# Performance work log

Hardware: AMD Instinct MI355X
Metric: run time of the kernel (lower is better)

The kernel has to match this reference:

```python
import jax, jax.numpy as jnp
import numpy as np

H = 128
B, N, K = 2, 16384, 16


def _gather_neighbors(a, idx):
    # a: (B,N,D), idx: (B,N,K) -> (B,N,K,D), per-batch gather along N
    return jax.vmap(lambda ab, ib: ab[ib])(a, idx)


def setup_inputs() -> dict:
    key = jax.random.key(0)
    ks = jax.random.split(key, 16)
    def lin(k, fan_in, shape):
        lim = 1.0 / np.sqrt(fan_in)
        return jax.random.uniform(k, shape, jnp.float32, -lim, lim)
    inp = {
        'h': jax.random.normal(ks[0], (B, N, H), jnp.float32),
        'x': jax.random.normal(ks[1], (B, N, 3), jnp.float32),
        'edge_idx': jax.random.randint(ks[2], (B, N, K), 0, N),
        # edge_mlp: Linear(2H+1->H), SiLU, Linear(H->H), SiLU
        'We1': lin(ks[3], 2 * H + 1, (2 * H + 1, H)), 'be1': lin(ks[4], 2 * H + 1, (H,)),
        'We2': lin(ks[5], H, (H, H)), 'be2': lin(ks[6], H, (H,)),
        # coord_mlp: Linear(H->H), SiLU, Linear(H->1, no bias)
        'Wc1': lin(ks[7], H, (H, H)), 'bc1': lin(ks[8], H, (H,)),
        'Wc2': lin(ks[9], H, (H, 1)),
        # node_mlp: Linear(2H->H), SiLU, Linear(H->H)
        'Wn1': lin(ks[10], 2 * H, (2 * H, H)), 'bn1': lin(ks[11], 2 * H, (H,)),
        'Wn2': lin(ks[12], H, (H, H)), 'bn2': lin(ks[13], H, (H,)),
    }
    return inp


def reference(h, x, edge_idx, We1, be1, We2, be2, Wc1, bc1, Wc2, Wn1, bn1, Wn2, bn2):
    k = edge_idx.shape[2]
    h_neigh = _gather_neighbors(h, edge_idx)          # (B,N,K,H)
    x_neigh = _gather_neighbors(x, edge_idx)          # (B,N,K,3)
    x_diff = x[:, :, None, :] - x_neigh               # (B,N,K,3)
    sq_dist = jnp.sum(x_diff * x_diff, axis=-1, keepdims=True)  # (B,N,K,1)
    h_i = jnp.broadcast_to(h[:, :, None, :], h_neigh.shape)
    edge_feat = jnp.concatenate([h_i, h_neigh, sq_dist], axis=-1)  # (B,N,K,2H+1)
    m_ij = jax.nn.silu(jax.nn.silu(edge_feat @ We1 + be1) @ We2 + be2)  # (B,N,K,H)
    coord_w = jax.nn.silu(m_ij @ Wc1 + bc1) @ Wc2     # (B,N,K,1)
    x_new = x + jnp.mean(x_diff * coord_w, axis=2)    # (B,N,3)
    m_i = jnp.sum(m_ij, axis=2)                       # (B,N,H)
    node_in = jnp.concatenate([h, m_i], axis=-1)      # (B,N,2H)
    h_new = jax.nn.silu(node_in @ Wn1 + bn1) @ Wn2 + bn2 + h
    return (h_new, x_new)
```

## Files before the change

### kernel.cpp

```cpp
#include <hip/hip_runtime.h>
#include <hip/hip_bf16.h>
#include <math.h>

#define H 128
#define KN 16
#define NN 16384
#define NB 8
#define EB 128
#define HS 136

typedef short s16x8 __attribute__((ext_vector_type(8)));
typedef float f32x4 __attribute__((ext_vector_type(4)));

__device__ __forceinline__ float u2f_lo(uint u){
    union { uint i; float f; } v; v.i = u << 16; return v.f;
}
__device__ __forceinline__ float u2f_hi(uint u){
    union { uint i; float f; } v; v.i = u & 0xffff0000u; return v.f;
}
__device__ __forceinline__ uint pk2(float lo, float hi){
    __hip_bfloat162 b = __float22bfloat162_rn(float2{lo, hi});
    uint u; __builtin_memcpy(&u, &b, 4); return u;
}
__device__ __forceinline__ ushort f2b1(float f){
    __hip_bfloat16 b = __float2bfloat16(f);
    ushort u; __builtin_memcpy(&u, &b, 2); return u;
}
__device__ __forceinline__ float silu_f(float v){
    float e = __expf(-v);
    return v * __builtin_amdgcn_rcpf(1.0f + e);
}

__global__ __launch_bounds__(256) void pack_all(
    const float* __restrict__ We2, const float* __restrict__ Wc1,
    const float* __restrict__ Wn1, const float* __restrict__ Wn2,
    const float* __restrict__ We1,
    ushort* __restrict__ dWe2, ushort* __restrict__ dWc1,
    ushort* __restrict__ dWn1, ushort* __restrict__ dWn2,
    ushort* __restrict__ dW1p)
{
    int idx = blockIdx.x * 256 + threadIdx.x;
    int fid = idx >> 6, l = idx & 63;
    const float* src; ushort* dst; int Kt; int mode = 0; int lfid;
    if (fid < 32)       { src = We2; dst = dWe2; Kt = 4; lfid = fid; }
    else if (fid < 64)  { src = Wc1; dst = dWc1; Kt = 4; lfid = fid - 32; }
    else if (fid < 128) { src = Wn1; dst = dWn1; Kt = 8; lfid = fid - 64; }
    else if (fid < 160) { src = Wn2; dst = dWn2; Kt = 4; lfid = fid - 128; }
    else                { src = We1; dst = dW1p; Kt = 4; mode = 1; lfid = fid - 160; }
    int mt = lfid / Kt, kt = lfid % Kt;
    int m = mt * 16 + (l & 15);
    s16x8 ov;
#pragma unroll
    for (int e = 0; e < 8; e++){
        int k = kt * 32 + ((l >> 4) << 3) + e;
        float v;
        if (mode == 0) v = src[k * 128 + m];
        else           v = src[(k + ((m >= 128) ? 128 : 0)) * 128 + (m & 127)];
        ov[e] = (short)f2b1(v);
    }
    *(s16x8*)(dst + (size_t)lfid * 512 + l * 8) = ov;
}

__global__ __launch_bounds__(256) void precompute_mfma(
    const float* __restrict__ h, const float* __restrict__ be1,
    const ushort* __restrict__ W1p,
    ushort* __restrict__ A, ushort* __restrict__ Bm)
{
    const int tid = threadIdx.x;
    const int w = tid >> 6, l = tid & 63, lg = l >> 4, li = l & 15;
    const int i0 = blockIdx.x * 64;

    f32x4 acc[4][4];
#pragma unroll
    for (int a = 0; a < 4; a++)
#pragma unroll
        for (int b = 0; b < 4; b++){ acc[a][b][0]=0.f; acc[a][b][1]=0.f; acc[a][b][2]=0.f; acc[a][b][3]=0.f; }

    for (int nt = 0; nt < 4; nt++){
        int node = i0 + nt * 16 + li;
        const float* hp = h + (size_t)node * 128 + lg * 8;
        s16x8 bfr[4];
#pragma unroll
        for (int kt = 0; kt < 4; kt++){
            float4 v0 = *(const float4*)(hp + kt * 32);
            float4 v1 = *(const float4*)(hp + kt * 32 + 4);
            uint4 uu = make_uint4(pk2(v0.x, v0.y), pk2(v0.z, v0.w),
                                  pk2(v1.x, v1.y), pk2(v1.z, v1.w));
            s16x8 bf; __builtin_memcpy(&bf, &uu, 16);
            bfr[kt] = bf;
        }
#pragma unroll
        for (int mtl = 0; mtl < 4; mtl++){
            int mt = w * 4 + mtl;
#pragma unroll
            for (int kt = 0; kt < 4; kt++){
                s16x8 af = *(const s16x8*)(W1p + (size_t)(mt * 4 + kt) * 512 + l * 8);
                acc[mtl][nt] = __builtin_amdgcn_mfma_f32_16x16x32_bf16(af, bfr[kt], acc[mtl][nt], 0, 0, 0);
            }
        }
    }
#pragma unroll
    for (int mtl = 0; mtl < 4; mtl++){
        int mt = w * 4 + mtl;
        int ccb = mt * 16 + lg * 4;
#pragma unroll
        for (int nt = 0; nt < 4; nt++){
            int node = i0 + nt * 16 + li;
            float b0=0.f,b1=0.f,b2=0.f,b3=0.f;
            if (ccb < 128){ float4 bb = *(const float4*)(be1 + ccb); b0=bb.x; b1=bb.y; b2=bb.z; b3=bb.w; }
            uint2 val = make_uint2(pk2(acc[mtl][nt][0] + b0, acc[mtl][nt][1] + b1),
                                   pk2(acc[mtl][nt][2] + b2, acc[mtl][nt][3] + b3));
            ushort* dst = (ccb < 128) ? (A + (size_t)node * 128 + ccb)
                                      : (Bm + (size_t)node * 128 + (ccb - 128));
            *(uint2*)dst = val;
        }
    }
}

__global__ __launch_bounds__(256, 3) void egnn_fused(
    const float* __restrict__ h, const float* __restrict__ x,
    const int* __restrict__ edge_idx,
    const ushort* __restrict__ A, const ushort* __restrict__ Bm,
    const float* __restrict__ We1,
    const ushort* __restrict__ We2T, const float* __restrict__ be2,
    const ushort* __restrict__ Wc1T, const float* __restrict__ bc1,
    const float* __restrict__ Wc2,
    const ushort* __restrict__ Wn1T, const float* __restrict__ bn1,
    const ushort* __restrict__ Wn2T, const float* __restrict__ bn2,
    float* __restrict__ out, int BN)
{
    __shared__ __align__(16) ushort m_lds[EB * 128];
    __shared__ __align__(16) uint   AshCw[512];
    __shared__ __align__(16) ushort hsh_bf[NB * HS];
    __shared__ __align__(16) ushort msum_bf[NB * HS];
    __shared__ __align__(16) ushort w256sh[128];
    __shared__ float  sqd[EB];
    __shared__ float  xd[EB * 3];
    __shared__ int    jgs[EB];

    ushort* Ash = (ushort*)AshCw;
    float (*cwvp)[EB] = (float(*)[EB])AshCw;

    const int tid = threadIdx.x;
    const int w = tid >> 6, l = tid & 63, lg = l >> 4, li = l & 15;
    const int i0 = blockIdx.x * NB;

    {
        int r = tid >> 5, c = (tid & 31) * 4;
        float4 hv = *(const float4*)&h[(size_t)(i0 + r) * 128 + c];
        *(uint2*)&hsh_bf[r * HS + c] = make_uint2(pk2(hv.x, hv.y), pk2(hv.z, hv.w));
        if (tid < 128){
            int rr = tid >> 4, cc = (tid & 15) * 8;
            *(uint4*)&Ash[rr * 128 + cc] = *(const uint4*)&A[(size_t)(i0 + rr) * 128 + cc];
        } else {
            int t2 = tid - 128;
            w256sh[t2] = f2b1(We1[256 * 128 + t2]);
        }
        if (tid < EB){
            int e = tid;
            int i = i0 + (e >> 4);
            int b = i / NN;
            int jl = edge_idx[(size_t)i * KN + (e & 15)];
            int j = b * NN + jl;
            jgs[e] = j;
            float d0 = x[(size_t)i*3+0] - x[(size_t)j*3+0];
            float d1 = x[(size_t)i*3+1] - x[(size_t)j*3+1];
            float d2 = x[(size_t)i*3+2] - x[(size_t)j*3+2];
            xd[e*3+0] = d0; xd[e*3+1] = d1; xd[e*3+2] = d2;
            sqd[e] = d0*d0 + d1*d1 + d2*d2;
        }
    }
    __syncthreads();

    {
        const int e0 = w * 32;
#pragma unroll
        for (int nt = 0; nt < 2; nt++){
            int edge = e0 + nt * 16 + li;
            int nodel = edge >> 4;
            int j = jgs[edge];
            float sq = sqd[edge];
#pragma unroll
            for (int kt = 0; kt < 4; kt++){
                int c8 = kt * 32 + lg * 8;
                uint4 ub = *(const uint4*)&Bm[(size_t)j * 128 + c8];
                uint4 ua = *(const uint4*)&Ash[nodel * 128 + c8];
                uint4 uw = *(const uint4*)&w256sh[c8];
                uint ov[4];
                const uint* pa = (const uint*)&ua;
                const uint* pb = (const uint*)&ub;
                const uint* pw = (const uint*)&uw;
#pragma unroll
                for (int p = 0; p < 4; p++){
                    float tlo = fmaf(sq, u2f_lo(pw[p]), u2f_lo(pa[p]) + u2f_lo(pb[p]));
                    float thi = fmaf(sq, u2f_hi(pw[p]), u2f_hi(pa[p]) + u2f_hi(pb[p]));
                    ov[p] = pk2(silu_f(tlo), silu_f(thi));
                }
                int blk = (kt * 4 + lg) ^ (edge & 7);
                *(uint4*)&m_lds[edge * 128 + blk * 8] = make_uint4(ov[0], ov[1], ov[2], ov[3]);
            }
        }
    }
    __syncthreads();

    f32x4 acc[16];
#pragma unroll
    for (int q = 0; q < 16; q++){ acc[q][0]=0.f; acc[q][1]=0.f; acc[q][2]=0.f; acc[q][3]=0.f; }

    __builtin_amdgcn_s_setprio(1);
#pragma unroll
    for (int kt = 0; kt < 4; kt++){
        s16x8 bfr[8];
#pragma unroll
        for (int nt = 0; nt < 8; nt++){
            int edge = nt * 16 + li;
            int blk = (kt * 4 + lg) ^ (edge & 7);
            bfr[nt] = *(const s16x8*)&m_lds[edge * 128 + blk * 8];
        }
#pragma unroll
        for (int mtl = 0; mtl < 2; mtl++){
            int mt = w * 2 + mtl;
            s16x8 af = *(const s16x8*)&We2T[(size_t)(mt * 4 + kt) * 512 + l * 8];
#pragma unroll
            for (int nt = 0; nt < 8; nt++)
                acc[mtl * 8 + nt] = __builtin_amdgcn_mfma_f32_16x16x32_bf16(af, bfr[nt], acc[mtl * 8 + nt], 0, 0, 0);
        }
    }
    __builtin_amdgcn_s_setprio(0);
    __syncthreads();

#pragma unroll
    for (int mtl = 0; mtl < 2; mtl++){
        int mt = w * 2 + mtl;
        int cb = mt * 16 + lg * 4;
        float4 bb = *(const float4*)&be2[cb];
#pragma unroll
        for (int nt = 0; nt < 8; nt++){
            int edge = nt * 16 + li;
            f32x4 a = acc[mtl * 8 + nt];
            uint2 val = make_uint2(pk2(silu_f(a[0] + bb.x), silu_f(a[1] + bb.y)),
                                   pk2(silu_f(a[2] + bb.z), silu_f(a[3] + bb.w)));
            int blk = (mt * 2 + (lg >> 1)) ^ (edge & 7);
            *(uint2*)&m_lds[edge * 128 + blk * 8 + (lg & 1) * 4] = val;
        }
    }
    __syncthreads();
    {
        int nodel = l >> 3;
        int c0 = w * 32 + (l & 7) * 4;
        float s0=0.f, s1=0.f, s2=0.f, s3=0.f;
#pragma unroll
        for (int k = 0; k < 16; k++){
            int edge = nodel * 16 + k;
            int blk = (c0 >> 3) ^ (edge & 7);
            uint2 v = *(uint2*)&m_lds[edge * 128 + blk * 8 + (c0 & 4)];
            s0 += u2f_lo(v.x); s1 += u2f_hi(v.x);
            s2 += u2f_lo(v.y); s3 += u2f_hi(v.y);
        }
        *(uint2*)&msum_bf[nodel * HS + c0] = make_uint2(pk2(s0, s1), pk2(s2, s3));
    }
    __syncthreads();

#pragma unroll
    for (int q = 0; q < 16; q++){ acc[q][0]=0.f; acc[q][1]=0.f; acc[q][2]=0.f; acc[q][3]=0.f; }
    __builtin_amdgcn_s_setprio(1);
#pragma unroll
    for (int kt = 0; kt < 4; kt++){
        s16x8 bfr[8];
#pragma unroll
        for (int nt = 0; nt < 8; nt++){
            int edge = nt * 16 + li;
            int blk = (kt * 4 + lg) ^ (edge & 7);
            bfr[nt] = *(const s16x8*)&m_lds[edge * 128 + blk * 8];
        }
#pragma unroll
        for (int mtl = 0; mtl < 2; mtl++){
            int mt = w * 2 + mtl;
            s16x8 af = *(const s16x8*)&Wc1T[(size_t)(mt * 4 + kt) * 512 + l * 8];
#pragma unroll
            for (int nt = 0; nt < 8; nt++)
                acc[mtl * 8 + nt] = __builtin_amdgcn_mfma_f32_16x16x32_bf16(af, bfr[nt], acc[mtl * 8 + nt], 0, 0, 0);
        }
    }
    __builtin_amdgcn_s_setprio(0);
    __syncthreads();

    {
        float cwp[8];
#pragma unroll
        for (int nt = 0; nt < 8; nt++) cwp[nt] = 0.f;
#pragma unroll
        for (int mtl = 0; mtl < 2; mtl++){
            int mt = w * 2 + mtl;
            int cb = mt * 16 + lg * 4;
            float4 bc = *(const float4*)&bc1[cb];
            float4 wc = *(const float4*)&Wc2[cb];
#pragma unroll
            for (int nt = 0; nt < 8; nt++){
                f32x4 a = acc[mtl * 8 + nt];
                cwp[nt] += silu_f(a[0] + bc.x) * wc.x + silu_f(a[1] + bc.y) * wc.y
                         + silu_f(a[2] + bc.z) * wc.z + silu_f(a[3] + bc.w) * wc.w;
            }
        }
#pragma unroll
        for (int nt = 0; nt < 8; nt++){
            float v = cwp[nt];
            v += __shfl_xor(v, 16);
            v += __shfl_xor(v, 32);
            if (lg == 0) cwvp[w][nt * 16 + li] = v;
        }
    }

    {
        f32x4 acc3[2];
        acc3[0][0]=0.f; acc3[0][1]=0.f; acc3[0][2]=0.f; acc3[0][3]=0.f;
        acc3[1][0]=0.f; acc3[1][1]=0.f; acc3[1][2]=0.f; acc3[1][3]=0.f;
        int node = li & 7;
#pragma unroll
        for (int kt = 0; kt < 8; kt++){
            const ushort* bp = (kt < 4) ? &hsh_bf[node * HS + kt * 32 + lg * 8]
                                        : &msum_bf[node * HS + (kt - 4) * 32 + lg * 8];
            s16x8 bf = *(const s16x8*)bp;
#pragma unroll
            for (int mtl = 0; mtl < 2; mtl++){
                int mt = w * 2 + mtl;
                s16x8 af = *(const s16x8*)&Wn1T[(size_t)(mt * 8 + kt) * 512 + l * 8];
                acc3[mtl] = __builtin_amdgcn_mfma_f32_16x16x32_bf16(af, bf, acc3[mtl], 0, 0, 0);
            }
        }
#pragma unroll
        for (int mtl = 0; mtl < 2; mtl++){
            int mt = w * 2 + mtl;
            int cb = mt * 16 + lg * 4;
            float4 bb = *(const float4*)&bn1[cb];
            uint o01 = 0, o23 = 0;
            if (li < 8){
                f32x4 a = acc3[mtl];
                o01 = pk2(silu_f(a[0] + bb.x), silu_f(a[1] + bb.y));
                o23 = pk2(silu_f(a[2] + bb.z), silu_f(a[3] + bb.w));
            }
            int blk = (mt * 2 + (lg >> 1)) ^ (li & 7);
            *(uint2*)&m_lds[li * 128 + blk * 8 + (lg & 1) * 4] = make_uint2(o01, o23);
        }
    }
    __syncthreads();

    if (tid < 24){
        int nd = tid / 3, d = tid % 3;
        int i = i0 + nd;
        float s = 0.f;
#pragma unroll
        for (int k = 0; k < 16; k++){
            int e = nd * 16 + k;
            float cw = cwvp[0][e] + cwvp[1][e] + cwvp[2][e] + cwvp[3][e];
            s += xd[e * 3 + d] * cw;
        }
        out[(size_t)BN * H + (size_t)i * 3 + d] = x[(size_t)i * 3 + d] + s * (1.0f / 16.0f);
    }

    {
        f32x4 acc4[2];
        acc4[0][0]=0.f; acc4[0][1]=0.f; acc4[0][2]=0.f; acc4[0][3]=0.f;
        acc4[1][0]=0.f; acc4[1][1]=0.f; acc4[1][2]=0.f; acc4[1][3]=0.f;
#pragma unroll
        for (int kt = 0; kt < 4; kt++){
            int blk = (kt * 4 + lg) ^ (li & 7);
            s16x8 bf = *(const s16x8*)&m_lds[li * 128 + blk * 8];
#pragma unroll
            for (int mtl = 0; mtl < 2; mtl++){
                int mt = w * 2 + mtl;
                s16x8 af = *(const s16x8*)&Wn2T[(size_t)(mt * 4 + kt) * 512 + l * 8];
                acc4[mtl] = __builtin_amdgcn_mfma_f32_16x16x32_bf16(af, bf, acc4[mtl], 0, 0, 0);
            }
        }
#pragma unroll
        for (int mtl = 0; mtl < 2; mtl++){
            int mt = w * 2 + mtl;
            int cb = mt * 16 + lg * 4;
            if (li < 8){
                float4 bb = *(const float4*)&bn2[cb];
                uint2 hu = *(const uint2*)&hsh_bf[li * HS + cb];
                f32x4 a = acc4[mtl];
                float4 o;
                o.x = a[0] + bb.x + u2f_lo(hu.x);
                o.y = a[1] + bb.y + u2f_hi(hu.x);
                o.z = a[2] + bb.z + u2f_lo(hu.y);
                o.w = a[3] + bb.w + u2f_hi(hu.y);
                *(float4*)&out[(size_t)(i0 + li) * 128 + cb] = o;
            }
        }
    }
}

extern "C" void kernel_launch(void* const* d_in, const int* in_sizes, int n_in,
                              void* d_out, int out_size, void* d_ws, size_t ws_size,
                              hipStream_t stream) {
    const float* h        = (const float*)d_in[0];
    const float* x        = (const float*)d_in[1];
    const int*   edge_idx = (const int*)d_in[2];
    const float* We1      = (const float*)d_in[3];
    const float* be1      = (const float*)d_in[4];
    const float* We2      = (const float*)d_in[5];
    const float* be2      = (const float*)d_in[6];
    const float* Wc1      = (const float*)d_in[7];
    const float* bc1      = (const float*)d_in[8];
    const float* Wc2      = (const float*)d_in[9];
    const float* Wn1      = (const float*)d_in[10];
    const float* bn1      = (const float*)d_in[11];
    const float* Wn2      = (const float*)d_in[12];
    const float* bn2      = (const float*)d_in[13];
    float* out = (float*)d_out;

    const int BN = in_sizes[0] / H;

    ushort* A    = (ushort*)d_ws;
    ushort* Bm   = A + (size_t)BN * H;
    ushort* We2T = Bm + (size_t)BN * H;
    ushort* Wc1T = We2T + 32 * 512;
    ushort* Wn1T = Wc1T + 32 * 512;
    ushort* Wn2T = Wn1T + 64 * 512;
    ushort* W1pT = Wn2T + 32 * 512;

    pack_all<<<56, 256, 0, stream>>>(We2, Wc1, Wn1, Wn2, We1,
                                     We2T, Wc1T, Wn1T, Wn2T, W1pT);
    precompute_mfma<<<BN / 64, 256, 0, stream>>>(h, be1, W1pT, A, Bm);
    egnn_fused<<<BN / NB, 256, 0, stream>>>(h, x, edge_idx, A, Bm, We1,
                                            We2T, be2, Wc1T, bc1, Wc2,
                                            Wn1T, bn1, Wn2T, bn2, out, BN);
}
```

Measured before the change: 125.1 us.

## Split edge GEMMs into half-width passes and shrink LDS to raise occupancy

```diff
diff --git a/kernel.cpp b/kernel.cpp
--- a/kernel.cpp
+++ b/kernel.cpp
@@ -17,6 +17,9 @@
 }
 __device__ __forceinline__ float u2f_hi(uint u){
     union { uint i; float f; } v; v.i = u & 0xffff0000u; return v.f;
+}
+__device__ __forceinline__ float b2f(ushort u){
+    union { uint i; float f; } v; v.i = ((uint)u) << 16; return v.f;
 }
 __device__ __forceinline__ uint pk2(float lo, float hi){
     __hip_bfloat162 b = __float22bfloat162_rn(float2{lo, hi});
@@ -117,7 +120,88 @@
     }
 }
 
-__global__ __launch_bounds__(256, 3) void egnn_fused(
+__device__ __forceinline__ void gemm_pass(
+    const ushort* mlds, const ushort* __restrict__ WT,
+    int nt0, int w, int l, int lg, int li, f32x4 acc[2][4])
+{
+#pragma unroll
+    for (int kt = 0; kt < 4; kt++){
+        s16x8 bfr[4];
+#pragma unroll
+        for (int n = 0; n < 4; n++){
+            int edge = (nt0 + n) * 16 + li;
+            int blk = (kt * 4 + lg) ^ (edge & 7);
+            bfr[n] = *(const s16x8*)&mlds[edge * 128 + blk * 8];
+        }
+#pragma unroll
+        for (int mtl = 0; mtl < 2; mtl++){
+            s16x8 af = *(const s16x8*)&WT[(size_t)((w * 2 + mtl) * 4 + kt) * 512 + l * 8];
+#pragma unroll
+            for (int n = 0; n < 4; n++)
+                acc[mtl][n] = __builtin_amdgcn_mfma_f32_16x16x32_bf16(af, bfr[n], acc[mtl][n], 0, 0, 0);
+        }
+    }
+}
+
+__device__ __forceinline__ void m_epi(
+    ushort* mlds, const float* __restrict__ be2,
+    int nt0, int w, int lg, int li, f32x4 acc[2][4])
+{
+#pragma unroll
+    for (int mtl = 0; mtl < 2; mtl++){
+        int mt = w * 2 + mtl;
+        int cb = mt * 16 + lg * 4;
+        float4 bb = *(const float4*)&be2[cb];
+#pragma unroll
+        for (int n = 0; n < 4; n++){
+            int el = (nt0 + n) * 16 + li;
+            f32x4 a = acc[mtl][n];
+            uint2 val = make_uint2(pk2(silu_f(a[0] + bb.x), silu_f(a[1] + bb.y)),
+                                   pk2(silu_f(a[2] + bb.z), silu_f(a[3] + bb.w)));
+            int blk = (mt * 2 + (lg >> 1)) ^ (el & 7);
+            *(uint2*)&mlds[el * 128 + blk * 8 + (lg & 1) * 4] = val;
+        }
+    }
+}
+
+__device__ __forceinline__ void gemm2_pass(
+    const ushort* mlds, const ushort* __restrict__ WT,
+    const float* __restrict__ bc1, const float* __restrict__ Wc2,
+    float* cwrow, int nt0, int w, int l, int lg, int li)
+{
+    f32x4 acc[2][4];
+#pragma unroll
+    for (int m = 0; m < 2; m++)
+#pragma unroll
+        for (int n = 0; n < 4; n++){ acc[m][n][0]=0.f; acc[m][n][1]=0.f; acc[m][n][2]=0.f; acc[m][n][3]=0.f; }
+
+    __builtin_amdgcn_s_setprio(1);
+    gemm_pass(mlds, WT, nt0, w, l, lg, li, acc);
+    __builtin_amdgcn_s_setprio(0);
+
+    float cwp[4] = {0.f, 0.f, 0.f, 0.f};
+#pragma unroll
+    for (int mtl = 0; mtl < 2; mtl++){
+        int cb = (w * 2 + mtl) * 16 + lg * 4;
+        float4 bc = *(const float4*)&bc1[cb];
+        float4 wc = *(const float4*)&Wc2[cb];
+#pragma unroll
+        for (int n = 0; n < 4; n++){
+            f32x4 a = acc[mtl][n];
+            cwp[n] += silu_f(a[0] + bc.x) * wc.x + silu_f(a[1] + bc.y) * wc.y
+                    + silu_f(a[2] + bc.z) * wc.z + silu_f(a[3] + bc.w) * wc.w;
+        }
+    }
+#pragma unroll
+    for (int n = 0; n < 4; n++){
+        float v = cwp[n];
+        v += __shfl_xor(v, 16);
+        v += __shfl_xor(v, 32);
+        if (lg == 0) cwrow[(nt0 + n) * 16 + li] = v;
+    }
+}
+
+__global__ __launch_bounds__(256, 4) void egnn_fused(
     const float* __restrict__ h, const float* __restrict__ x,
     const int* __restrict__ edge_idx,
     const ushort* __restrict__ A, const ushort* __restrict__ Bm,
@@ -135,8 +219,8 @@
     __shared__ __align__(16) ushort msum_bf[NB * HS];
     __shared__ __align__(16) ushort w256sh[128];
     __shared__ float  sqd[EB];
-    __shared__ float  xd[EB * 3];
-    __shared__ int    jgs[EB];
+    __shared__ ushort xdb[EB * 3];
+    __shared__ ushort jgs[EB];
 
     ushort* Ash = (ushort*)AshCw;
     float (*cwvp)[EB] = (float(*)[EB])AshCw;
@@ -162,11 +246,11 @@
             int b = i / NN;
             int jl = edge_idx[(size_t)i * KN + (e & 15)];
             int j = b * NN + jl;
-            jgs[e] = j;
+            jgs[e] = (ushort)j;
             float d0 = x[(size_t)i*3+0] - x[(size_t)j*3+0];
             float d1 = x[(size_t)i*3+1] - x[(size_t)j*3+1];
             float d2 = x[(size_t)i*3+2] - x[(size_t)j*3+2];
-            xd[e*3+0] = d0; xd[e*3+1] = d1; xd[e*3+2] = d2;
+            xdb[e*3+0] = f2b1(d0); xdb[e*3+1] = f2b1(d1); xdb[e*3+2] = f2b1(d2);
             sqd[e] = d0*d0 + d1*d1 + d2*d2;
         }
     }
@@ -203,57 +287,41 @@
     }
     __syncthreads();
 
-    f32x4 acc[16];
-#pragma unroll
-    for (int q = 0; q < 16; q++){ acc[q][0]=0.f; acc[q][1]=0.f; acc[q][2]=0.f; acc[q][3]=0.f; }
-
-    __builtin_amdgcn_s_setprio(1);
-#pragma unroll
-    for (int kt = 0; kt < 4; kt++){
-        s16x8 bfr[8];
-#pragma unroll
-        for (int nt = 0; nt < 8; nt++){
-            int edge = nt * 16 + li;
-            int blk = (kt * 4 + lg) ^ (edge & 7);
-            bfr[nt] = *(const s16x8*)&m_lds[edge * 128 + blk * 8];
-        }
-#pragma unroll
-        for (int mtl = 0; mtl < 2; mtl++){
-            int mt = w * 2 + mtl;
-            s16x8 af = *(const s16x8*)&We2T[(size_t)(mt * 4 + kt) * 512 + l * 8];
-#pragma unroll
-            for (int nt = 0; nt < 8; nt++)
-                acc[mtl * 8 + nt] = __builtin_amdgcn_mfma_f32_16x16x32_bf16(af, bfr[nt], acc[mtl * 8 + nt], 0, 0, 0);
-        }
-    }
-    __builtin_amdgcn_s_setprio(0);
-    __syncthreads();
-
-#pragma unroll
-    for (int mtl = 0; mtl < 2; mtl++){
-        int mt = w * 2 + mtl;
-        int cb = mt * 16 + lg * 4;
-        float4 bb = *(const float4*)&be2[cb];
-#pragma unroll
-        for (int nt = 0; nt < 8; nt++){
-            int edge = nt * 16 + li;
-            f32x4 a = acc[mtl * 8 + nt];
-            uint2 val = make_uint2(pk2(silu_f(a[0] + bb.x), silu_f(a[1] + bb.y)),
-                                   pk2(silu_f(a[2] + bb.z), silu_f(a[3] + bb.w)));
-            int blk = (mt * 2 + (lg >> 1)) ^ (edge & 7);
-            *(uint2*)&m_lds[edge * 128 + blk * 8 + (lg & 1) * 4] = val;
-        }
-    }
-    __syncthreads();
+    {
+        f32x4 acc[2][4];
+#pragma unroll
+        for (int m = 0; m < 2; m++)
+#pragma unroll
+            for (int n = 0; n < 4; n++){ acc[m][n][0]=0.f; acc[m][n][1]=0.f; acc[m][n][2]=0.f; acc[m][n][3]=0.f; }
+        __builtin_amdgcn_s_setprio(1);
+        gemm_pass(m_lds, We2T, 0, w, l, lg, li, acc);
+        __builtin_amdgcn_s_setprio(0);
+        __syncthreads();
+        m_epi(m_lds, be2, 0, w, lg, li, acc);
+    }
+    {
+        f32x4 acc[2][4];
+#pragma unroll
+        for (int m = 0; m < 2; m++)
+#pragma unroll
+            for (int n = 0; n < 4; n++){ acc[m][n][0]=0.f; acc[m][n][1]=0.f; acc[m][n][2]=0.f; acc[m][n][3]=0.f; }
+        __builtin_amdgcn_s_setprio(1);
+        gemm_pass(m_lds, We2T, 4, w, l, lg, li, acc);
+        __builtin_amdgcn_s_setprio(0);
+        __syncthreads();
+        m_epi(m_lds, be2, 4, w, lg, li, acc);
+    }
+
     {
         int nodel = l >> 3;
         int c0 = w * 32 + (l & 7) * 4;
         float s0=0.f, s1=0.f, s2=0.f, s3=0.f;
 #pragma unroll
-        for (int k = 0; k < 16; k++){
+        for (int s = 0; s < 16; s++){
+            int k = (s + nodel) & 15;
             int edge = nodel * 16 + k;
             int blk = (c0 >> 3) ^ (edge & 7);
-            uint2 v = *(uint2*)&m_lds[edge * 128 + blk * 8 + (c0 & 4)];
+            uint2 v = *(const uint2*)&m_lds[edge * 128 + blk * 8 + (c0 & 4)];
             s0 += u2f_lo(v.x); s1 += u2f_hi(v.x);
             s2 += u2f_lo(v.y); s3 += u2f_hi(v.y);
         }
@@ -261,55 +329,9 @@
     }
     __syncthreads();
 
-#pragma unroll
-    for (int q = 0; q < 16; q++){ acc[q][0]=0.f; acc[q][1]=0.f; acc[q][2]=0.f; acc[q][3]=0.f; }
-    __builtin_amdgcn_s_setprio(1);
-#pragma unroll
-    for (int kt = 0; kt < 4; kt++){
-        s16x8 bfr[8];
-#pragma unroll
-        for (int nt = 0; nt < 8; nt++){
-            int edge = nt * 16 + li;
-            int blk = (kt * 4 + lg) ^ (edge & 7);
-            bfr[nt] = *(const s16x8*)&m_lds[edge * 128 + blk * 8];
-        }
-#pragma unroll
-        for (int mtl = 0; mtl < 2; mtl++){
-            int mt = w * 2 + mtl;
-            s16x8 af = *(const s16x8*)&Wc1T[(size_t)(mt * 4 + kt) * 512 + l * 8];
-#pragma unroll
-            for (int nt = 0; nt < 8; nt++)
-                acc[mtl * 8 + nt] = __builtin_amdgcn_mfma_f32_16x16x32_bf16(af, bfr[nt], acc[mtl * 8 + nt], 0, 0, 0);
-        }
-    }
-    __builtin_amdgcn_s_setprio(0);
+    gemm2_pass(m_lds, Wc1T, bc1, Wc2, cwvp[w], 0, w, l, lg, li);
+    gemm2_pass(m_lds, Wc1T, bc1, Wc2, cwvp[w], 4, w, l, lg, li);
     __syncthreads();
-
-    {
-        float cwp[8];
-#pragma unroll
-        for (int nt = 0; nt < 8; nt++) cwp[nt] = 0.f;
-#pragma unroll
-        for (int mtl = 0; mtl < 2; mtl++){
-            int mt = w * 2 + mtl;
-            int cb = mt * 16 + lg * 4;
-            float4 bc = *(const float4*)&bc1[cb];
-            float4 wc = *(const float4*)&Wc2[cb];
-#pragma unroll
-            for (int nt = 0; nt < 8; nt++){
-                f32x4 a = acc[mtl * 8 + nt];
-                cwp[nt] += silu_f(a[0] + bc.x) * wc.x + silu_f(a[1] + bc.y) * wc.y
-                         + silu_f(a[2] + bc.z) * wc.z + silu_f(a[3] + bc.w) * wc.w;
-            }
-        }
-#pragma unroll
-        for (int nt = 0; nt < 8; nt++){
-            float v = cwp[nt];
-            v += __shfl_xor(v, 16);
-            v += __shfl_xor(v, 32);
-            if (lg == 0) cwvp[w][nt * 16 + li] = v;
-        }
-    }
 
     {
         f32x4 acc3[2];
@@ -353,7 +375,7 @@
         for (int k = 0; k < 16; k++){
             int e = nd * 16 + k;
             float cw = cwvp[0][e] + cwvp[1][e] + cwvp[2][e] + cwvp[3][e];
-            s += xd[e * 3 + d] * cw;
+            s += b2f(xdb[e * 3 + d]) * cw;
         }
         out[(size_t)BN * H + (size_t)i * 3 + d] = x[(size_t)i * 3 + d] + s * (1.0f / 16.0f);
     }
```

Result: faster. 119.8 us (median of 2 runs) (-4.2%).
